# Kernel tuning notes

Measured on AMD Instinct MI355X. Metric: run time of the kernel, lower is better.

## Reference

```python
import jax, jax.numpy as jnp
import numpy as np

S, B, E, H, Q, T, K, N = 256, 32, 768, 1024, 64, 512, 11, 16
STD = 2.5
EPS = 1e-5


def gaussian_kernel(size, std):
    t = np.linspace(-(size - 1) / 2, (size - 1) / 2, size)
    x, y = np.meshgrid(t, t)
    kern = np.exp(-0.5 * (x ** 2 + y ** 2) / std ** 2)
    return (kern / kern.sum()).astype(np.float32)


def setup_inputs() -> dict:
    key = jax.random.key(0)
    ks = jax.random.split(key, 24)
    s = 0.05
    inp = {
        'sentence_batch': jax.random.normal(ks[0], (S, B, E), jnp.float32),
        # forward LSTM params (torch layout: W_ih (4H,E), W_hh (4H,H), gate order i,f,g,o)
        'Wih_f': jax.random.normal(ks[1], (4 * H, E), jnp.float32) * s,
        'Whh_f': jax.random.normal(ks[2], (4 * H, H), jnp.float32) * s,
        'bih_f': jnp.zeros((4 * H,), jnp.float32),
        'bhh_f': jnp.zeros((4 * H,), jnp.float32),
        # backward LSTM params
        'Wih_b': jax.random.normal(ks[3], (4 * H, E), jnp.float32) * s,
        'Whh_b': jax.random.normal(ks[4], (4 * H, H), jnp.float32) * s,
        'bih_b': jnp.zeros((4 * H,), jnp.float32),
        'bhh_b': jnp.zeros((4 * H,), jnp.float32),
        # layer norms
        'g_in': jnp.ones((E,), jnp.float32), 'be_in': jnp.zeros((E,), jnp.float32),
        'g_fw': jnp.ones((H,), jnp.float32), 'be_fw': jnp.zeros((H,), jnp.float32),
        'g_bk': jnp.ones((H,), jnp.float32), 'be_bk': jnp.zeros((H,), jnp.float32),
        'g_sq': jnp.ones((2 * Q,), jnp.float32), 'be_sq': jnp.zeros((2 * Q,), jnp.float32),
        # squeeze + topic linears (torch layout: W (out,in))
        'Wsq': jax.random.normal(ks[5], (Q, H), jnp.float32) * s,
        'bsq': jnp.zeros((Q,), jnp.float32),
        'Wtop': jax.random.normal(ks[6], (T, 2 * Q), jnp.float32) * s,
        'btop': jnp.zeros((T,), jnp.float32),
        'gauss_kern': jnp.asarray(gaussian_kernel(K, STD)),
    }
    return inp


def layer_norm(x, g, b):
    mu = jnp.mean(x, axis=-1, keepdims=True)
    var = jnp.mean((x - mu) ** 2, axis=-1, keepdims=True)
    return g * (x - mu) * jax.lax.rsqrt(var + EPS) + b


def lstm(x, Wih, Whh, bih, bhh):
    # x: (S, B, E) -> hidden states (S, B, H). torch gate order: i, f, g, o.
    h0 = jnp.zeros((x.shape[1], Whh.shape[1]), x.dtype)
    c0 = jnp.zeros_like(h0)
    xg = jnp.einsum('sbe,ge->sbg', x, Wih) + bih  # precompute input gates

    def step(carry, xt):
        h, c = carry
        gates = xt + h @ Whh.T + bhh
        i, f, g, o = jnp.split(gates, 4, axis=-1)
        c = jax.nn.sigmoid(f) * c + jax.nn.sigmoid(i) * jnp.tanh(g)
        h = jax.nn.sigmoid(o) * jnp.tanh(c)
        return (h, c), h

    _, hs = jax.lax.scan(step, (h0, c0), xg)
    return hs


def batch_pca(e, dim):
    # e: (S, B, F) -> projections (B, S, dim) onto top-dim principal axes
    c = e - jnp.mean(e, axis=0)
    cov = jnp.einsum('sbi,sbj->bij', c, c) / e.shape[0]  # (B, F, F), symmetric
    _, evecs = jnp.linalg.eigh(cov)  # ascending eigenvalues
    top = evecs[:, :, ::-1][:, :, :dim]  # (B, F, dim), descending order
    return jnp.einsum('sbf,bfn->bsn', c, top)


def gauss_smooth(x, kern):
    # x: (B, S, N) smoothed with 2D gaussian, SAME padding
    p = (kern.shape[0] - 1) // 2
    y = jax.lax.conv_general_dilated(
        x[:, None, :, :], kern[None, None, :, :], (1, 1), [(p, p), (p, p)])
    return y[:, 0]


def adj_cos(e):
    # cosine similarity between adjacent sequence positions: (B, S, N) -> (B, S-1)
    a, b = e[:, :-1], e[:, 1:]
    num = jnp.sum(a * b, axis=-1)
    den = jnp.linalg.norm(a, axis=-1) * jnp.linalg.norm(b, axis=-1)
    return num / den


def reference(sentence_batch, Wih_f, Whh_f, bih_f, bhh_f, Wih_b, Whh_b, bih_b, bhh_b,
              g_in, be_in, g_fw, be_fw, g_bk, be_bk, g_sq, be_sq,
              Wsq, bsq, Wtop, btop, gauss_kern):
    x = layer_norm(sentence_batch, g_in, be_in)
    x_f = lstm(x, Wih_f, Whh_f, bih_f, bhh_f)
    x_b = lstm(x[::-1], Wih_b, Whh_b, bih_b, bhh_b)[::-1]
    x_f = layer_norm(x_f, g_fw, be_fw)
    x_b = layer_norm(x_b, g_bk, be_bk)
    x_f = jnp.tanh(jnp.einsum('sbh,qh->sbq', x_f, Wsq) + bsq)
    x_b = jnp.tanh(jnp.einsum('sbh,qh->sbq', x_b, Wsq) + bsq)
    xc = layer_norm(jnp.concatenate((x_f, x_b), axis=-1), g_sq, be_sq)
    topic_preds = jnp.einsum('sbq,tq->sbt', xc, Wtop) + btop

    # segmentation path (no-grad in original)
    e_f = batch_pca(jax.lax.stop_gradient(x_f), N)
    e_b = batch_pca(jax.lax.stop_gradient(x_b), N)
    e_f = gauss_smooth(e_f, gauss_kern)
    e_b = gauss_smooth(e_b, gauss_kern)
    d = jnp.sqrt(adj_cos(e_f) * adj_cos(e_b))  # (B, S-1)
    pos = jnp.argmax(d, axis=1)
    return topic_preds, pos
```

## Files before the change

kernel.cpp:

```cpp
#include <hip/hip_runtime.h>
#include <cstdint>
#include <cstddef>

#define SS   256
#define BB   32
#define EE   768
#define HH   1024
#define QQ   64
#define TTOP 512
#define NPC  16
#define G4   4096
#define TCHUNK 32
#define NBLK 256
#define EPSF 1e-5f

#define OFF_XNT   ((size_t)0)
#define OFF_WHHT  ((size_t)6291456)
#define OFF_CT    ((size_t)14680064)
#define OFF_HBUF  ((size_t)14745600)
#define OFF_CNT   ((size_t)14876672)
#define OFF_XG    ((size_t)14877184)
#define OFF_HS    ((size_t)23265792)
#define OFF_XQ    ((size_t)40043008)
#define OFF_CMAT  ((size_t)0)
#define OFF_COV   ((size_t)1048576)
#define OFF_PG    ((size_t)1310720)
#define OFF_COS   ((size_t)1376256)

#define WLKS 4616
#define LSTM_DYN_LDS 153344

#define AST 65
#define EIG_DYN_LDS 133120

#define EPS32D    5.9604644775390625e-8
#define EPS232D   (EPS32D*EPS32D)
#define SAFMIN32D 1.1754943508222875e-38

__device__ __forceinline__ float sigm(float x){ return 1.0f/(1.0f + expf(-x)); }

__device__ __forceinline__ double wsumd(double v){
  #pragma unroll
  for (int o = 32; o; o >>= 1) v += __shfl_xor(v, o, 64);
  return v;
}
__device__ __forceinline__ double wmaxd(double v){
  #pragma unroll
  for (int o = 32; o; o >>= 1) v = fmax(v, __shfl_xor(v, o, 64));
  return v;
}
__device__ __forceinline__ void dlartg_(double f, double g, double& c, double& s, double& r){
  if (g == 0.0){ c = 1.0; s = 0.0; r = f; }
  else if (f == 0.0){ c = 0.0; s = (g >= 0.0) ? 1.0 : -1.0; r = fabs(g); }
  else {
    double d = sqrt(f*f + g*g);
    c = fabs(f)/d;
    r = copysign(d, f);
    s = g/r;
  }
}
__device__ void dlaev2_(double a, double b, double c,
                        double& rt1, double& rt2, double& cs1, double& sn1){
  double sm = a + c, df = a - c, adf = fabs(df), tb = b + b, ab = fabs(tb);
  double acmx, acmn;
  if (fabs(a) > fabs(c)){ acmx = a; acmn = c; } else { acmx = c; acmn = a; }
  double rt;
  if (adf > ab)      rt = adf*sqrt(1.0 + (ab/adf)*(ab/adf));
  else if (adf < ab) rt = ab*sqrt(1.0 + (adf/ab)*(adf/ab));
  else               rt = ab*sqrt(2.0);
  int sgn1;
  if (sm < 0.0){ rt1 = 0.5*(sm - rt); sgn1 = -1; rt2 = (acmx/rt1)*acmn - (b/rt1)*b; }
  else if (sm > 0.0){ rt1 = 0.5*(sm + rt); sgn1 = 1; rt2 = (acmx/rt1)*acmn - (b/rt1)*b; }
  else { rt1 = 0.5*rt; rt2 = -0.5*rt; sgn1 = 1; }
  double cs; int sgn2;
  if (df >= 0.0){ cs = df + rt; sgn2 = 1; } else { cs = df - rt; sgn2 = -1; }
  double acs = fabs(cs);
  if (acs > ab){ double ct = -tb/cs; sn1 = 1.0/sqrt(1.0+ct*ct); cs1 = ct*sn1; }
  else {
    if (ab == 0.0){ cs1 = 1.0; sn1 = 0.0; }
    else { double tn = -cs/tb; cs1 = 1.0/sqrt(1.0+tn*tn); sn1 = tn*cs1; }
  }
  if (sgn1 == sgn2){ double tn = cs1; cs1 = -sn1; sn1 = tn; }
}

__device__ void dsteqr16_(int base, double* d, double* e, double* z16, int ln){
  if (ln < 16){
    #pragma unroll
    for (int j = 0; j < 16; j++) z16[ln*17+j] = (ln==j) ? 1.0 : 0.0;
  }
  __syncthreads();
  const int n = 16, nm1 = 15;
  int jtot = 0; const int nmaxit = 480;
  int l1 = 0;
  while (l1 < n){
    if (l1 > 0) e[base+l1-1] = 0.0;
    int m = nm1;
    for (int mm = l1; mm < nm1; mm++){
      double tst = fabs(e[base+mm]);
      if (tst == 0.0){ m = mm; break; }
      if (tst <= (sqrt(fabs(d[base+mm]))*sqrt(fabs(d[base+mm+1])))*EPS32D){
        e[base+mm] = 0.0; m = mm; break;
      }
    }
    int l = l1, lend = m;
    l1 = m + 1;
    if (lend == l) continue;
    if (fabs(d[base+lend]) < fabs(d[base+l])){ int t = l; l = lend; lend = t; }
    if (lend > l){
      for (;;){
        int mm = lend;
        for (int k2 = l; k2 < lend; k2++){
          double tst = e[base+k2]*e[base+k2];
          if (tst <= (EPS232D*fabs(d[base+k2]))*fabs(d[base+k2+1]) + SAFMIN32D){ mm = k2; break; }
        }
        if (mm < lend) e[base+mm] = 0.0;
        double p = d[base+l];
        if (mm == l){ l++; if (l <= lend) continue; break; }
        if (mm == l+1){
          double rt1, rt2, cc, ss;
          dlaev2_(d[base+l], e[base+l], d[base+l+1], rt1, rt2, cc, ss);
          if (ln < 16){
            double x = z16[ln*17+l], y = z16[ln*17+l+1];
            z16[ln*17+l]   = cc*x + ss*y;
            z16[ln*17+l+1] = cc*y - ss*x;
          }
          d[base+l] = rt1; d[base+l+1] = rt2; e[base+l] = 0.0;
          l += 2; if (l <= lend) continue; break;
        }
        if (jtot == nmaxit) break;
        jtot++;
        double g = (d[base+l+1]-p)/(2.0*e[base+l]);
        double r = sqrt(g*g+1.0);
        g = d[base+mm] - p + e[base+l]/(g + copysign(r, g));
        double s2 = 1.0, c2 = 1.0; p = 0.0;
        for (int i = mm-1; i >= l; i--){
          double f = s2*e[base+i], b = c2*e[base+i];
          dlartg_(g, f, c2, s2, r);
          if (i != mm-1) e[base+i+1] = r;
          g = d[base+i+1] - p;
          r = (d[base+i]-g)*s2 + 2.0*c2*b;
          p = s2*r;
          d[base+i+1] = g + p;
          g = c2*r - b;
          if (ln < 16){
            double x = z16[ln*17+i], y = z16[ln*17+i+1];
            z16[ln*17+i]   = c2*x - s2*y;
            z16[ln*17+i+1] = s2*x + c2*y;
          }
        }
        d[base+l] -= p; e[base+l] = g;
      }
    } else {
      for (;;){
        int mm = lend;
        for (int k2 = l; k2 > lend; k2--){
          double tst = e[base+k2-1]*e[base+k2-1];
          if (tst <= (EPS232D*fabs(d[base+k2]))*fabs(d[base+k2-1]) + SAFMIN32D){ mm = k2; break; }
        }
        if (mm > lend) e[base+mm-1] = 0.0;
        double p = d[base+l];
        if (mm == l){ l--; if (l >= lend) continue; break; }
        if (mm == l-1){
          double rt1, rt2, cc, ss;
          dlaev2_(d[base+l-1], e[base+l-1], d[base+l], rt1, rt2, cc, ss);
          if (ln < 16){
            double x = z16[ln*17+l-1], y = z16[ln*17+l];
            z16[ln*17+l-1] = cc*x + ss*y;
            z16[ln*17+l]   = cc*y - ss*x;
          }
          d[base+l-1] = rt1; d[base+l] = rt2; e[base+l-1] = 0.0;
          l -= 2; if (l >= lend) continue; break;
        }
        if (jtot == nmaxit) break;
        jtot++;
        double g = (d[base+l-1]-p)/(2.0*e[base+l-1]);
        double r = sqrt(g*g+1.0);
        g = d[base+mm] - p + e[base+l-1]/(g + copysign(r, g));
        double s2 = 1.0, c2 = 1.0; p = 0.0;
        for (int i = mm; i <= l-1; i++){
          double f = s2*e[base+i], b = c2*e[base+i];
          dlartg_(g, f, c2, s2, r);
          if (i != mm) e[base+i-1] = r;
          g = d[base+i] - p;
          r = (d[base+i+1]-g)*s2 + 2.0*c2*b;
          p = s2*r;
          d[base+i] = g + p;
          g = c2*r - b;
          if (ln < 16){
            double x = z16[ln*17+i], y = z16[ln*17+i+1];
            z16[ln*17+i]   = c2*x + s2*y;
            z16[ln*17+i+1] = c2*y - s2*x;
          }
        }
        d[base+l] -= p; e[base+l-1] = g;
      }
    }
  }
  for (int ii = 1; ii < n; ii++){
    int i = ii-1, k = i; double p = d[base+i];
    for (int j = ii; j < n; j++) if (d[base+j] < p){ k = j; p = d[base+j]; }
    if (k != i){
      d[base+k] = d[base+i]; d[base+i] = p;
      if (ln < 16){ double t = z16[ln*17+i]; z16[ln*17+i] = z16[ln*17+k]; z16[ln*17+k] = t; }
    }
  }
  __syncthreads();
}

__device__ void dc_merge(int base, int n1, int n2, double rho_in, int ln,
    double* s_d, double* Zt, double* Tt,
    double* md, double* mz, double* dl, double* wz, double* lam, double* zh,
    double* ev, double* su, int* indx, int* sec, int* defl, int* prm){
  int n = n1 + n2;
  double zv = 0.0;
  if (ln < n){
    if (ln < n1) zv = Zt[(size_t)(base+n1-1)*AST + base + ln];
    else         zv = Zt[(size_t)(base+n1)*AST + base + ln];
    if (rho_in < 0.0 && ln >= n1) zv = -zv;
  }
  zv *= 0.70710678118654752440;
  mz[ln] = (ln < n) ? zv : 0.0;
  md[ln] = (ln < n) ? s_d[base+ln] : 0.0;
  __syncthreads();
  double rho = fabs(2.0*rho_in);
  if (ln == 0){
    int i1 = 0, i2 = n1, k = 0;
    while (i1 < n1 && i2 < n){
      if (md[i2] < md[i1]) indx[k++] = i2++; else indx[k++] = i1++;
    }
    while (i1 < n1) indx[k++] = i1++;
    while (i2 < n)  indx[k++] = i2++;
  }
  __syncthreads();
  double dmax = wmaxd((ln<n) ? fabs(md[ln]) : 0.0);
  double zmax = wmaxd((ln<n) ? fabs(mz[ln]) : 0.0);
  double tol = 8.0*EPS32D*fmax(dmax, zmax);
  int K = 0, ndefl = 0, pj = -1;
  for (int j = 0; j < n; j++){
    int nj = indx[j];
    if (rho*fabs(mz[nj]) <= tol){
      defl[ndefl++] = nj;
    } else if (pj < 0){
      pj = nj;
    } else {
      double sG = mz[pj], cG = mz[nj];
      double tau = sqrt(cG*cG + sG*sG);
      double tdf = md[nj] - md[pj];
      double c = cG/tau, s = -sG/tau;
      if (fabs(tdf*c*s) <= tol){
        mz[nj] = tau; mz[pj] = 0.0;
        if (ln < n){
          double x = Zt[(size_t)(base+ln)*AST + base+pj];
          double y = Zt[(size_t)(base+ln)*AST + base+nj];
          Zt[(size_t)(base+ln)*AST + base+pj] = c*x + s*y;
          Zt[(size_t)(base+ln)*AST + base+nj] = c*y - s*x;
        }
        __syncthreads();
        double t2 = md[pj]*c*c + md[nj]*s*s;
        double t3 = md[pj]*s*s + md[nj]*c*c;
        md[nj] = t3; md[pj] = t2;
        defl[ndefl++] = pj;
        pj = nj;
      } else {
        sec[K] = pj; dl[K] = md[pj]; wz[K] = mz[pj]; K++;
        pj = nj;
      }
    }
  }
  if (pj >= 0){ sec[K] = pj; dl[K] = md[pj]; wz[K] = mz[pj]; K++; }
  __syncthreads();
  double wsum2 = wsumd((ln < K) ? wz[ln]*wz[ln] : 0.0);
  if (ln < K){
    double lo = dl[ln];
    double hi = (ln < K-1) ? dl[ln+1] : (dl[K-1] + rho*wsum2);
    for (int it = 0; it < 120; it++){
      double mid = 0.5*(lo+hi);
      if (!(mid > lo) || !(mid < hi)) break;
      double fv = 1.0;
      for (int i2 = 0; i2 < K; i2++) fv += rho*wz[i2]*wz[i2]/(dl[i2]-mid);
      if (fv < 0.0) lo = mid; else hi = mid;
    }
    double lj = 0.5*(lo+hi);
    if (!(lj > dl[ln])) lj = nextafter(dl[ln], 1.0e300);
    lam[ln] = lj;
  }
  __syncthreads();
  if (ln < K){
    double di = dl[ln];
    double prod = lam[K-1] - di;
    for (int j2 = 0; j2 < ln; j2++)   prod *= (lam[j2]-di)/(dl[j2]-di);
    for (int j2 = ln; j2 < K-1; j2++) prod *= (lam[j2]-di)/(dl[j2+1]-di);
    zh[ln] = copysign(sqrt(fabs(prod)), wz[ln]);
  }
  __syncthreads();
  for (int j = 0; j < K; j++){
    double ui = (ln < K) ? zh[ln]/(dl[ln]-lam[j]) : 0.0;
    double nrm = sqrt(wsumd(ui*ui));
    su[ln] = ui/nrm;
    __syncthreads();
    if (ln < n){
      double acc = 0.0;
      for (int i2 = 0; i2 < K; i2++)
        acc += Zt[(size_t)(base+ln)*AST + base + sec[i2]]*su[i2];
      Tt[(size_t)ln*AST + j] = acc;
    }
    if (ln == 0) ev[j] = lam[j];
    __syncthreads();
  }
  for (int j = 0; j < ndefl; j++){
    int cj = defl[j];
    if (ln < n) Tt[(size_t)ln*AST + K + j] = Zt[(size_t)(base+ln)*AST + base + cj];
    if (ln == 0) ev[K+j] = md[cj];
  }
  __syncthreads();
  if (ln == 0){
    for (int i2 = 0; i2 < n; i2++) prm[i2] = i2;
    for (int a2 = 0; a2 < n-1; a2++){
      int kk = a2;
      for (int b2 = a2+1; b2 < n; b2++) if (ev[prm[b2]] < ev[prm[kk]]) kk = b2;
      int t3 = prm[a2]; prm[a2] = prm[kk]; prm[kk] = t3;
    }
  }
  __syncthreads();
  if (ln < n){
    for (int c2 = 0; c2 < n; c2++)
      Zt[(size_t)(base+ln)*AST + base + c2] = Tt[(size_t)ln*AST + prm[c2]];
  }
  if (ln == 0){ for (int c2 = 0; c2 < n; c2++) s_d[base+c2] = ev[prm[c2]]; }
  __syncthreads();
}

__global__ __launch_bounds__(64) void k_eig(const float* __restrict__ covg,
                                            float* __restrict__ Pg){
  int u = blockIdx.x, ln = threadIdx.x;
  extern __shared__ double dsm[];
  double* A  = dsm;
  double* Qh = dsm + 4160;
  double* Zt = dsm + 8320;
  double* Tt = dsm + 12480;
  __shared__ double s_d[64], s_e[64], s_tau[64], s_v[64], s_w[64];
  __shared__ double md[64], mz[64], dl[64], wz[64], lam[64], zh[64], ev[64], su[64];
  __shared__ double z16[16*17];
  __shared__ int indx[64], sec[64], defl[64], prm[64];

  for (int n = ln; n < 4096; n += 64)
    A[(n >> 6)*AST + (n & 63)] = (double)covg[(size_t)u*4096 + n];
  __syncthreads();

  for (int i = 0; i < 63; i++){
    double alpha = A[(size_t)(i+1)*AST + i];
    double xv = (ln >= i+2) ? A[(size_t)ln*AST + i] : 0.0;
    double xnorm2 = wsumd(xv*xv);
    if (xnorm2 == 0.0){
      if (ln == 0){ s_e[i] = alpha; s_tau[i] = 0.0; }
    } else {
      double beta = -copysign(sqrt(alpha*alpha + xnorm2), alpha);
      double taui = (beta - alpha)/beta;
      double sc = 1.0/(alpha - beta);
      s_v[ln] = (ln == i+1) ? 1.0 : ((ln >= i+2) ? A[(size_t)ln*AST+i]*sc : 0.0);
      __syncthreads();
      if (ln >= i+2) A[(size_t)ln*AST+i] = s_v[ln];
      double wr = 0.0;
      if (ln >= i+1){
        for (int c2 = i+1; c2 < 64; c2++){
          double av = (ln >= c2) ? A[(size_t)ln*AST+c2] : A[(size_t)c2*AST+ln];
          wr += av*s_v[c2];
        }
        wr *= taui;
      }
      double dotwv = wsumd((ln >= i+1) ? wr*s_v[ln] : 0.0);
      double alp2 = -0.5*taui*dotwv;
      wr += alp2*s_v[ln];
      s_w[ln] = (ln >= i+1) ? wr : 0.0;
      __syncthreads();
      if (ln >= i+1){
        for (int c2 = i+1; c2 <= ln; c2++)
          A[(size_t)ln*AST+c2] -= s_v[ln]*s_w[c2] + s_w[ln]*s_v[c2];
      }
      if (ln == 0){ s_e[i] = beta; s_tau[i] = taui; }
    }
    __syncthreads();
  }
  s_d[ln] = A[(size_t)ln*AST+ln];
  __syncthreads();

  for (int n = ln; n < 4160; n += 64) Qh[n] = 0.0;
  __syncthreads();
  Qh[(size_t)ln*AST+ln] = 1.0;
  __syncthreads();
  for (int i = 62; i >= 0; i--){
    double taui = s_tau[i];
    if (taui != 0.0){
      s_v[ln] = (ln == i+1) ? 1.0 : ((ln >= i+2) ? A[(size_t)ln*AST+i] : 0.0);
      __syncthreads();
      double dj = 0.0;
      for (int r2 = i+1; r2 < 64; r2++) dj += s_v[r2]*Qh[(size_t)r2*AST+ln];
      dj *= taui;
      for (int r2 = i+1; r2 < 64; r2++) Qh[(size_t)r2*AST+ln] -= s_v[r2]*dj;
    }
    __syncthreads();
  }

  double rho_a = s_e[15], rho_b = s_e[47], rho_top = s_e[31];
  if (ln == 0){
    s_d[15] -= fabs(rho_a);   s_d[16] -= fabs(rho_a);
    s_d[31] -= fabs(rho_top); s_d[32] -= fabs(rho_top);
    s_d[47] -= fabs(rho_b);   s_d[48] -= fabs(rho_b);
  }
  for (int n = ln; n < 4160; n += 64) Zt[n] = 0.0;
  __syncthreads();
  for (int leaf = 0; leaf < 4; leaf++){
    dsteqr16_(leaf*16, s_d, s_e, z16, ln);
    if (ln < 16){
      for (int j = 0; j < 16; j++)
        Zt[(size_t)(leaf*16+ln)*AST + leaf*16 + j] = z16[ln*17+j];
    }
    __syncthreads();
  }
  dc_merge(0, 16, 16, rho_a, ln, s_d, Zt, Tt, md, mz, dl, wz, lam, zh, ev, su, indx, sec, defl, prm);
  dc_merge(32, 16, 16, rho_b, ln, s_d, Zt, Tt, md, mz, dl, wz, lam, zh, ev, su, indx, sec, defl, prm);
  dc_merge(0, 32, 32, rho_top, ln, s_d, Zt, Tt, md, mz, dl, wz, lam, zh, ev, su, indx, sec, defl, prm);

  for (int nn = 0; nn < 16; nn++){
    double acc = 0.0;
    for (int k = 0; k < 64; k++)
      acc += Qh[(size_t)ln*AST+k]*Zt[(size_t)k*AST + (63-nn)];
    Pg[(size_t)u*1024 + ln*16 + nn] = (float)acc;
  }
}

__global__ void k_ln_in(const float* __restrict__ x, const float* __restrict__ g,
                        const float* __restrict__ be, float* __restrict__ xnT){
  int bid = blockIdx.x; int s = bid >> 5, b = bid & 31;
  int tid = threadIdx.x;
  const float* row = x + ((size_t)(s*BB + b))*EE;
  __shared__ float r1[256], r2[256];
  float su = 0.f, sq = 0.f;
  for (int e = tid; e < EE; e += 256){ float v = row[e]; su += v; sq += v*v; }
  r1[tid] = su; r2[tid] = sq; __syncthreads();
  for (int st = 128; st > 0; st >>= 1){
    if (tid < st){ r1[tid] += r1[tid+st]; r2[tid] += r2[tid+st]; }
    __syncthreads();
  }
  float mu  = r1[0] * (1.0f/EE);
  float var = r2[0] * (1.0f/EE) - mu*mu;
  float rstd = rsqrtf(var + EPSF);
  for (int e = tid; e < EE; e += 256){
    float v = (row[e]-mu)*rstd*g[e] + be[e];
    xnT[((size_t)s*EE + e)*BB + b] = v;
  }
}

__global__ void k_whht(const float* __restrict__ Whh_f, const float* __restrict__ Whh_b,
                       float* __restrict__ WhhT){
  int d  = blockIdx.z;
  const float* Whh = d ? Whh_b : Whh_f;
  int rt = blockIdx.x*32, kt = blockIdx.y*32;
  int tx = threadIdx.x & 31, ty = threadIdx.x >> 5;
  __shared__ float tile[32][33];
  for (int i = ty; i < 32; i += 8)
    tile[i][tx] = Whh[(size_t)(rt+i)*HH + kt+tx];
  __syncthreads();
  for (int i = ty; i < 32; i += 8)
    WhhT[((size_t)d*HH + kt+i)*G4 + rt+tx] = tile[tx][i];
}

__global__ void k_zero(float* __restrict__ p, int n){
  int i = blockIdx.x*blockDim.x + threadIdx.x;
  if (i < n) p[i] = 0.f;
}

__global__ __launch_bounds__(256) void k_xg(const float* __restrict__ xnT,
        const float* __restrict__ Wih_f, const float* __restrict__ Wih_b,
        float* __restrict__ xg, int* __restrict__ cnt, int c){
  if (blockIdx.x == 0 && blockIdx.y == 0 && threadIdx.x < 17)
    __hip_atomic_store(&cnt[threadIdx.x*16], 0, __ATOMIC_RELAXED, __HIP_MEMORY_SCOPE_AGENT);
  int nb = blockIdx.x, rb = blockIdx.y;
  int d = rb >> 5, rloc0 = (rb & 31)*128;
  const float* Wih = d ? Wih_b : Wih_f;
  int tid = threadIdx.x;
  int tx = tid & 15, ty = tid >> 4;
  __shared__ float Al[16*132];
  __shared__ float Bl[16*132];
  float acc[8][8];
  #pragma unroll
  for (int i = 0; i < 8; i++)
    #pragma unroll
    for (int j = 0; j < 8; j++) acc[i][j] = 0.f;
  for (int kc = 0; kc < EE; kc += 16){
    #pragma unroll
    for (int j = 0; j < 8; j++){
      int idx = tid + j*256;
      int n = idx & 127, k = idx >> 7;
      int tglob = c*TCHUNK + nb*4 + (n >> 5);
      int tsrc = d ? (SS-1-tglob) : tglob;
      Al[k*132 + n] = xnT[((size_t)tsrc*EE + kc + k)*BB + (n & 31)];
    }
    #pragma unroll
    for (int j = 0; j < 8; j++){
      int idx = tid + j*256;
      int k = idx & 15, r = idx >> 4;
      Bl[k*132 + r] = Wih[(size_t)(rloc0 + r)*EE + kc + k];
    }
    __syncthreads();
    #pragma unroll
    for (int k = 0; k < 16; k++){
      float4 a0 = *(const float4*)(&Al[k*132 + tx*4]);
      float4 a1 = *(const float4*)(&Al[k*132 + 64 + tx*4]);
      float4 b0 = *(const float4*)(&Bl[k*132 + ty*4]);
      float4 b1 = *(const float4*)(&Bl[k*132 + 64 + ty*4]);
      float av[8] = {a0.x,a0.y,a0.z,a0.w,a1.x,a1.y,a1.z,a1.w};
      float bv[8] = {b0.x,b0.y,b0.z,b0.w,b1.x,b1.y,b1.z,b1.w};
      #pragma unroll
      for (int i = 0; i < 8; i++)
        #pragma unroll
        for (int j2 = 0; j2 < 8; j2++) acc[i][j2] += av[i]*bv[j2];
    }
    __syncthreads();
  }
  #pragma unroll
  for (int j = 0; j < 8; j++){
    int r = rloc0 + ((j < 4) ? (ty*4 + j) : (64 + ty*4 + j - 4));
    #pragma unroll
    for (int ig = 0; ig < 2; ig++){
      int n0 = ig*64 + tx*4;
      int tl = nb*4 + (n0 >> 5), b = n0 & 31;
      float4 o = make_float4(acc[ig*4+0][j], acc[ig*4+1][j], acc[ig*4+2][j], acc[ig*4+3][j]);
      *(float4*)(&xg[(((size_t)tl*8192) + d*G4 + r)*BB + b]) = o;
    }
  }
}

__global__ __launch_bounds__(512) void k_lstm(
    const float* __restrict__ WhhT,
    const float* __restrict__ bih_f, const float* __restrict__ bhh_f,
    const float* __restrict__ bih_b, const float* __restrict__ bhh_b,
    const float* __restrict__ xg, float* __restrict__ hbuf,
    float* __restrict__ cT, float* __restrict__ hs,
    int* __restrict__ cnt, int c)
{
  extern __shared__ float lsm[];
  float* Wl  = lsm;
  float* gl  = lsm + 36928;
  float* cls = lsm + 38080;

  const int blk = blockIdx.x;
  const int d   = blk >> 7;
  const int j0  = (blk & 127) * 8;
  const int tid = threadIdx.x;
  const int ln  = tid & 63;
  const int w   = tid >> 6;
  const int ksub = ln >> 3;
  const int bg   = ln & 7;
  const int b0   = bg * 4;
  const int cbase = w * 4;

  const float* bih = d ? bih_b : bih_f;
  const float* bhh = d ? bhh_b : bhh_f;
  const float* WT_d = WhhT + (size_t)d * HH * G4;

  {
    const int cs = tid & 31;
    const int ks = tid >> 5;
    const int g  = cs >> 3, jj = cs & 7;
    const size_t rglob = (size_t)g*HH + j0 + jj;
    for (int kk = 0; kk < 64; kk++){
      int k = kk*16 + ks;
      Wl[(k >> 7)*WLKS + (k & 127)*36 + cs] = WT_d[(size_t)k*G4 + rglob];
    }
  }

  const int pjj = (tid >> 5) & 7, pb = tid & 31;
  float pbias[4];
  if (tid < 256){
    cls[pjj*32 + pb] = cT[((size_t)d*HH + j0 + pjj)*BB + pb];
    #pragma unroll
    for (int g2 = 0; g2 < 4; g2++)
      pbias[g2] = bih[g2*HH + j0 + pjj] + bhh[g2*HH + j0 + pjj];
  }
  __syncthreads();

  for (int tl = 0; tl < TCHUNK; tl++){
    const int s = c*TCHUNK + tl;
    const float* hprev = hbuf + ((size_t)((s & 1)*2 + d))*HH*BB;
    float*       hnext = hbuf + ((size_t)(((s+1) & 1)*2 + d))*HH*BB;

    float xgv[4] = {0.f,0.f,0.f,0.f};
    if (tid < 256){
      const size_t xbase = ((size_t)tl*8192 + (size_t)d*G4)*BB;
      #pragma unroll
      for (int g2 = 0; g2 < 4; g2++)
        xgv[g2] = xg[xbase + (size_t)(g2*HH + j0 + pjj)*BB + pb];
    }

    float acc[4][4];
    #pragma unroll
    for (int i = 0; i < 4; i++)
      #pragma unroll
      for (int j = 0; j < 4; j++) acc[i][j] = 0.f;

    {
      const float* hp = hprev + (size_t)(ksub*128)*BB + b0;
      const float* wrow = &Wl[ksub*WLKS + cbase];
      for (int ib = 0; ib < 128; ib += 16){
        float4 hv[16];
        #pragma unroll
        for (int u = 0; u < 16; u++)
          hv[u] = *(const float4*)(hp + (size_t)(ib+u)*BB);
        #pragma unroll
        for (int u = 0; u < 16; u++){
          float4 wv = *(const float4*)(wrow + (ib+u)*36);
          acc[0][0] += wv.x*hv[u].x; acc[0][1] += wv.x*hv[u].y; acc[0][2] += wv.x*hv[u].z; acc[0][3] += wv.x*hv[u].w;
          acc[1][0] += wv.y*hv[u].x; acc[1][1] += wv.y*hv[u].y; acc[1][2] += wv.y*hv[u].z; acc[1][3] += wv.y*hv[u].w;
          acc[2][0] += wv.z*hv[u].x; acc[2][1] += wv.z*hv[u].y; acc[2][2] += wv.z*hv[u].z; acc[2][3] += wv.z*hv[u].w;
          acc[3][0] += wv.w*hv[u].x; acc[3][1] += wv.w*hv[u].y; acc[3][2] += wv.w*hv[u].z; acc[3][3] += wv.w*hv[u].w;
        }
      }
    }
    #pragma unroll
    for (int i = 0; i < 4; i++)
      #pragma unroll
      for (int j = 0; j < 4; j++){
        float v = acc[i][j];
        v += __shfl_xor(v, 8, 64);
        v += __shfl_xor(v, 16, 64);
        v += __shfl_xor(v, 32, 64);
        acc[i][j] = v;
      }
    if (ksub == 0){
      #pragma unroll
      for (int i = 0; i < 4; i++){
        float4 o = make_float4(acc[i][0], acc[i][1], acc[i][2], acc[i][3]);
        *(float4*)(&gl[(cbase + i)*36 + b0]) = o;
      }
    }
    __syncthreads();
    if (tid < 256){
      float gv[4];
      #pragma unroll
      for (int g2 = 0; g2 < 4; g2++)
        gv[g2] = gl[(g2*8 + pjj)*36 + pb] + pbias[g2] + xgv[g2];
      float iv = sigm(gv[0]), fv = sigm(gv[1]), ggv = tanhf(gv[2]), ov = sigm(gv[3]);
      float cv = fv*cls[pjj*32 + pb] + iv*ggv;
      cls[pjj*32 + pb] = cv;
      float h = ov*tanhf(cv);
      hnext[(size_t)(j0 + pjj)*BB + pb] = h;
      int tsv = d ? (SS-1-s) : s;
      hs[(((size_t)d*SS + tsv)*HH + j0 + pjj)*BB + pb] = h;
    }
    if (tl < TCHUNK-1){
      __syncthreads();
      if (tid == 0){
        __builtin_amdgcn_fence(__ATOMIC_RELEASE, "agent");
        __hip_atomic_fetch_add(&cnt[(blk & 15)*16], 1, __ATOMIC_RELAXED, __HIP_MEMORY_SCOPE_AGENT);
        const int target = 16*(tl+1);
        if (blk == 0){
          int done = 0;
          while (done < 16){
            done = 0;
            #pragma unroll
            for (int i = 0; i < 16; i++)
              done += (__hip_atomic_load(&cnt[i*16], __ATOMIC_RELAXED, __HIP_MEMORY_SCOPE_AGENT) >= target);
            if (done < 16) __builtin_amdgcn_s_sleep(2);
          }
          __hip_atomic_store(&cnt[256], tl+1, __ATOMIC_RELAXED, __HIP_MEMORY_SCOPE_AGENT);
        } else {
          while (__hip_atomic_load(&cnt[256], __ATOMIC_RELAXED, __HIP_MEMORY_SCOPE_AGENT) < tl+1)
            __builtin_amdgcn_s_sleep(2);
        }
        __builtin_amdgcn_fence(__ATOMIC_ACQUIRE, "agent");
      }
      __syncthreads();
    }
  }
  __syncthreads();
  if (tid < 256)
    cT[((size_t)d*HH + j0 + pjj)*BB + pb] = cls[pjj*32 + pb];
}

__global__ __launch_bounds__(256) void k_lnproj(const float* __restrict__ hs,
        const float* __restrict__ g_fw, const float* __restrict__ be_fw,
        const float* __restrict__ g_bk, const float* __restrict__ be_bk,
        const float* __restrict__ Wsq, const float* __restrict__ bsq,
        float* __restrict__ xq){
  int t = blockIdx.x, d = blockIdx.y;
  int tid = threadIdx.x;
  const float* gv  = d ? g_bk  : g_fw;
  const float* bev = d ? be_bk : be_fw;
  const float* hrow = hs + ((size_t)d*SS + t)*HH*BB;
  __shared__ float red[256], red2[256];
  __shared__ float smu[32], srs[32];
  __shared__ float ln[32*132];
  __shared__ float wl[64*132];
  {
    int b = tid & 31, jg = tid >> 5;
    float s = 0.f, s2 = 0.f;
    for (int j = jg*128; j < jg*128+128; j++){
      float v = hrow[(size_t)j*BB + b];
      s += v; s2 += v*v;
    }
    red[b*8 + jg] = s; red2[b*8 + jg] = s2; __syncthreads();
    if (tid < 32){
      float a = 0.f, a2 = 0.f;
      for (int k = 0; k < 8; k++){ a += red[tid*8+k]; a2 += red2[tid*8+k]; }
      float mu = a*(1.f/HH), var = a2*(1.f/HH) - mu*mu;
      smu[tid] = mu; srs[tid] = rsqrtf(var + EPSF);
    }
    __syncthreads();
  }
  float acc[4][2] = {{0.f,0.f},{0.f,0.f},{0.f,0.f},{0.f,0.f}};
  int qg = tid & 31, bg = tid >> 5;
  int q0 = qg*2, b0g = bg*4;
  for (int jc = 0; jc < 8; jc++){
    for (int n = tid; n < 4096; n += 256){
      int b = n & 31, jj = n >> 5; int j = jc*128 + jj;
      float v = hrow[(size_t)j*BB + b];
      ln[b*132+jj] = (v - smu[b])*srs[b]*gv[j] + bev[j];
    }
    for (int n = tid; n < 8192; n += 256){
      int q = n >> 7, jj = n & 127;
      wl[q*132+jj] = Wsq[(size_t)q*HH + jc*128 + jj];
    }
    __syncthreads();
    for (int jj = 0; jj < 128; jj += 4){
      float4 w0 = *(const float4*)(&wl[q0*132+jj]);
      float4 w1 = *(const float4*)(&wl[(q0+1)*132+jj]);
      #pragma unroll
      for (int i = 0; i < 4; i++){
        float4 xv = *(const float4*)(&ln[(b0g+i)*132+jj]);
        acc[i][0] += xv.x*w0.x + xv.y*w0.y + xv.z*w0.z + xv.w*w0.w;
        acc[i][1] += xv.x*w1.x + xv.y*w1.y + xv.z*w1.z + xv.w*w1.w;
      }
    }
    __syncthreads();
  }
  #pragma unroll
  for (int i = 0; i < 4; i++)
    #pragma unroll
    for (int u = 0; u < 2; u++){
      float o = tanhf(acc[i][u] + bsq[q0+u]);
      xq[(((size_t)d*SS + t)*BB + (b0g+i))*QQ + q0 + u] = o;
    }
}

__global__ __launch_bounds__(256) void k_topic(const float* __restrict__ xq,
        const float* __restrict__ g_sq, const float* __restrict__ be_sq,
        const float* __restrict__ Wtop, const float* __restrict__ btop,
        float* __restrict__ out){
  int t = blockIdx.x; int tid = threadIdx.x;
  __shared__ float xc[32*132];
  __shared__ float wl[16*520];
  __shared__ float red[256], red2[256];
  __shared__ float smu[32], srs[32];
  for (int n = tid; n < 4096; n += 256){
    int b = n >> 7, q = n & 127;
    float v = (q < 64) ? xq[(((size_t)0*SS + t)*BB + b)*QQ + q]
                       : xq[(((size_t)1*SS + t)*BB + b)*QQ + (q-64)];
    xc[b*132+q] = v;
  }
  __syncthreads();
// ... 147 lines not shown
}

__global__ void k_pos(const float* __restrict__ cosb, float* __restrict__ out){
  __shared__ float mx[256];
  __shared__ int   mi[256];
  int tid = threadIdx.x;
  for (int b = 0; b < 32; b++){
    float v = -1e30f;
    if (tid < 255){
      float cf = cosb[(size_t)(b)*256 + tid];
      float cb = cosb[(size_t)(32+b)*256 + tid];
      v = sqrtf(cf*cb);
      if (isnan(v)) v = INFINITY;
    }
    mx[tid] = v; __syncthreads();
    for (int st = 128; st > 0; st >>= 1){
      if (tid < st) mx[tid] = fmaxf(mx[tid], mx[tid+st]);
      __syncthreads();
    }
    float m = mx[0]; __syncthreads();
    mi[tid] = (tid < 255 && v == m) ? tid : (1<<30);
    __syncthreads();
    for (int st = 128; st > 0; st >>= 1){
      if (tid < st) mi[tid] = min(mi[tid], mi[tid+st]);
      __syncthreads();
    }
    if (tid == 0) out[(size_t)SS*BB*TTOP + b] = (float)mi[0];
    __syncthreads();
  }
}

extern "C" void kernel_launch(void* const* d_in, const int* in_sizes, int n_in,
                              void* d_out, int out_size, void* d_ws, size_t ws_size,
                              hipStream_t stream){
  (void)in_sizes; (void)n_in; (void)out_size; (void)ws_size;
  const float* x      = (const float*)d_in[0];
  const float* Wih_f  = (const float*)d_in[1];
  const float* Whh_f  = (const float*)d_in[2];
  const float* bih_f  = (const float*)d_in[3];
  const float* bhh_f  = (const float*)d_in[4];
  const float* Wih_b  = (const float*)d_in[5];
  const float* Whh_b  = (const float*)d_in[6];
  const float* bih_b  = (const float*)d_in[7];
  const float* bhh_b  = (const float*)d_in[8];
  const float* g_in   = (const float*)d_in[9];
  const float* be_in  = (const float*)d_in[10];
  const float* g_fw   = (const float*)d_in[11];
  const float* be_fw  = (const float*)d_in[12];
  const float* g_bk   = (const float*)d_in[13];
  const float* be_bk  = (const float*)d_in[14];
  const float* g_sq   = (const float*)d_in[15];
  const float* be_sq  = (const float*)d_in[16];
  const float* Wsq    = (const float*)d_in[17];
  const float* bsq    = (const float*)d_in[18];
  const float* Wtop   = (const float*)d_in[19];
  const float* btop   = (const float*)d_in[20];
  const float* gkern  = (const float*)d_in[21];

  float* ws    = (float*)d_ws;
  float* xnT   = ws + OFF_XNT;
  float* WhhT  = ws + OFF_WHHT;
  float* cT    = ws + OFF_CT;
  float* hbuf  = ws + OFF_HBUF;
  int*   cnt   = (int*)(ws + OFF_CNT);
  float* xg    = ws + OFF_XG;
  float* hs    = ws + OFF_HS;
  float* xq    = ws + OFF_XQ;
  float* cmat  = ws + OFF_CMAT;
  float* covg  = ws + OFF_COV;
  float* Pg    = ws + OFF_PG;
  float* cosb  = ws + OFF_COS;
  float* out   = (float*)d_out;

  hipFuncSetAttribute((const void*)k_eig,
                      hipFuncAttributeMaxDynamicSharedMemorySize, EIG_DYN_LDS);
  hipFuncSetAttribute((const void*)k_lstm,
                      hipFuncAttributeMaxDynamicSharedMemorySize, LSTM_DYN_LDS);

  k_zero<<<dim3(768), dim3(256), 0, stream>>>(cT, 196608);
  k_ln_in<<<dim3(SS*BB), dim3(256), 0, stream>>>(x, g_in, be_in, xnT);
  k_whht<<<dim3(128, 32, 2), dim3(256), 0, stream>>>(Whh_f, Whh_b, WhhT);
  for (int c = 0; c < SS/TCHUNK; c++){
    k_xg<<<dim3(8, 64), dim3(256), 0, stream>>>(xnT, Wih_f, Wih_b, xg, cnt, c);
    k_lstm<<<dim3(NBLK), dim3(512), LSTM_DYN_LDS, stream>>>(WhhT, bih_f, bhh_f, bih_b, bhh_b,
                                                            xg, hbuf, cT, hs, cnt, c);
  }
  k_lnproj<<<dim3(SS,2), dim3(256), 0, stream>>>(hs, g_fw, be_fw, g_bk, be_bk, Wsq, bsq, xq);
  k_topic<<<dim3(SS), dim3(256), 0, stream>>>(xq, g_sq, be_sq, Wtop, btop, out);
  k_pca1<<<dim3(64), dim3(256), 0, stream>>>(xq, cmat, covg);
  k_eig<<<dim3(64), dim3(64), EIG_DYN_LDS, stream>>>(covg, Pg);
  k_pca2<<<dim3(64), dim3(256), 0, stream>>>(cmat, Pg, gkern, cosb);
  k_pos<<<dim3(1), dim3(256), 0, stream>>>(cosb, out);
}
```

Baseline: 8.312 ms.

## Restructure LSTM recurrence to 256 threads and parallelize eigensolver across four waves

The LSTM step kernel drops from 512 to 256 threads. Each wave now covers a 256-wide k-range for all 32 gate columns, and partial sums are combined through an LDS tree reduction instead of cross-lane shuffles, so the idle upper half of the block during the gate update goes away. The eigen kernel moves from 64 to 256 threads: the four 16x16 leaf QR solves run concurrently, one per wave, the secular-vector columns in the merge step are split across waves, and the Householder updates are split across waves by column. The trade-offs are fewer threads hiding latency in the LSTM and extra barriers in the reduction.

```diff
diff --git a/kernel.cpp b/kernel.cpp
--- a/kernel.cpp
+++ b/kernel.cpp
@@ -28,7 +28,7 @@
 #define OFF_COS   ((size_t)1376256)
 
 #define WLKS 4616
-#define LSTM_DYN_LDS 153344
+#define LSTM_DYN_LDS 161536
 
 #define AST 65
 #define EIG_DYN_LDS 133120
@@ -88,7 +88,6 @@
     #pragma unroll
     for (int j = 0; j < 16; j++) z16[ln*17+j] = (ln==j) ? 1.0 : 0.0;
   }
-  __syncthreads();
   const int n = 16, nm1 = 15;
   int jtot = 0; const int nmaxit = 480;
   int l1 = 0;
@@ -204,13 +203,14 @@
       if (ln < 16){ double t = z16[ln*17+i]; z16[ln*17+i] = z16[ln*17+k]; z16[ln*17+k] = t; }
     }
   }
-  __syncthreads();
-}
-
-__device__ void dc_merge(int base, int n1, int n2, double rho_in, int ln,
+}
+
+__device__ void dc_merge(int base, int n1, int n2, double rho_in, int tid,
     double* s_d, double* Zt, double* Tt,
     double* md, double* mz, double* dl, double* wz, double* lam, double* zh,
-    double* ev, double* su, int* indx, int* sec, int* defl, int* prm){
+    double* ev, double* su4, int* indx, int* sec, int* defl, int* prm,
+    int* sKn){
+  const int ln = tid & 63, w = tid >> 6;
   int n = n1 + n2;
   double zv = 0.0;
   if (ln < n){
@@ -223,7 +223,7 @@
   md[ln] = (ln < n) ? s_d[base+ln] : 0.0;
   __syncthreads();
   double rho = fabs(2.0*rho_in);
-  if (ln == 0){
+  if (tid == 0){
     int i1 = 0, i2 = n1, k = 0;
     while (i1 < n1 && i2 < n){
       if (md[i2] < md[i1]) indx[k++] = i2++; else indx[k++] = i1++;
@@ -235,40 +235,43 @@
   double dmax = wmaxd((ln<n) ? fabs(md[ln]) : 0.0);
   double zmax = wmaxd((ln<n) ? fabs(mz[ln]) : 0.0);
   double tol = 8.0*EPS32D*fmax(dmax, zmax);
-  int K = 0, ndefl = 0, pj = -1;
-  for (int j = 0; j < n; j++){
-    int nj = indx[j];
-    if (rho*fabs(mz[nj]) <= tol){
-      defl[ndefl++] = nj;
-    } else if (pj < 0){
-      pj = nj;
-    } else {
-      double sG = mz[pj], cG = mz[nj];
-      double tau = sqrt(cG*cG + sG*sG);
-      double tdf = md[nj] - md[pj];
-      double c = cG/tau, s = -sG/tau;
-      if (fabs(tdf*c*s) <= tol){
-        mz[nj] = tau; mz[pj] = 0.0;
-        if (ln < n){
-          double x = Zt[(size_t)(base+ln)*AST + base+pj];
-          double y = Zt[(size_t)(base+ln)*AST + base+nj];
-          Zt[(size_t)(base+ln)*AST + base+pj] = c*x + s*y;
-          Zt[(size_t)(base+ln)*AST + base+nj] = c*y - s*x;
-        }
-        __syncthreads();
-        double t2 = md[pj]*c*c + md[nj]*s*s;
-        double t3 = md[pj]*s*s + md[nj]*c*c;
-        md[nj] = t3; md[pj] = t2;
-        defl[ndefl++] = pj;
+  if (w == 0){
+    int K = 0, ndefl = 0, pj = -1;
+    for (int j = 0; j < n; j++){
+      int nj = indx[j];
+      if (rho*fabs(mz[nj]) <= tol){
+        defl[ndefl++] = nj;
+      } else if (pj < 0){
         pj = nj;
       } else {
-        sec[K] = pj; dl[K] = md[pj]; wz[K] = mz[pj]; K++;
-        pj = nj;
-      }
-    }
-  }
-  if (pj >= 0){ sec[K] = pj; dl[K] = md[pj]; wz[K] = mz[pj]; K++; }
-  __syncthreads();
+        double sG = mz[pj], cG = mz[nj];
+        double tau = sqrt(cG*cG + sG*sG);
+        double tdf = md[nj] - md[pj];
+        double c = cG/tau, s = -sG/tau;
+        if (fabs(tdf*c*s) <= tol){
+          mz[nj] = tau; mz[pj] = 0.0;
+          if (ln < n){
+            double x = Zt[(size_t)(base+ln)*AST + base+pj];
+            double y = Zt[(size_t)(base+ln)*AST + base+nj];
+            Zt[(size_t)(base+ln)*AST + base+pj] = c*x + s*y;
+            Zt[(size_t)(base+ln)*AST + base+nj] = c*y - s*x;
+          }
+          double t2 = md[pj]*c*c + md[nj]*s*s;
+          double t3 = md[pj]*s*s + md[nj]*c*c;
+          md[nj] = t3; md[pj] = t2;
+          defl[ndefl++] = pj;
+          pj = nj;
+        } else {
+          sec[K] = pj; dl[K] = md[pj]; wz[K] = mz[pj]; K++;
+          pj = nj;
+        }
+      }
+    }
+    if (pj >= 0){ sec[K] = pj; dl[K] = md[pj]; wz[K] = mz[pj]; K++; }
+    if (ln == 0){ sKn[0] = K; sKn[1] = ndefl; }
+  }
+  __syncthreads();
+  const int K = sKn[0], ndefl = sKn[1];
   double wsum2 = wsumd((ln < K) ? wz[ln]*wz[ln] : 0.0);
   if (ln < K){
     double lo = dl[ln];
@@ -293,27 +296,26 @@
     zh[ln] = copysign(sqrt(fabs(prod)), wz[ln]);
   }
   __syncthreads();
-  for (int j = 0; j < K; j++){
+  for (int j = w; j < K; j += 4){
     double ui = (ln < K) ? zh[ln]/(dl[ln]-lam[j]) : 0.0;
     double nrm = sqrt(wsumd(ui*ui));
-    su[ln] = ui/nrm;
-    __syncthreads();
+    su4[w*64 + ln] = ui/nrm;
     if (ln < n){
       double acc = 0.0;
       for (int i2 = 0; i2 < K; i2++)
-        acc += Zt[(size_t)(base+ln)*AST + base + sec[i2]]*su[i2];
+        acc += Zt[(size_t)(base+ln)*AST + base + sec[i2]]*su4[w*64 + i2];
       Tt[(size_t)ln*AST + j] = acc;
     }
     if (ln == 0) ev[j] = lam[j];
-    __syncthreads();
-  }
+  }
+  __syncthreads();
   for (int j = 0; j < ndefl; j++){
     int cj = defl[j];
     if (ln < n) Tt[(size_t)ln*AST + K + j] = Zt[(size_t)(base+ln)*AST + base + cj];
     if (ln == 0) ev[K+j] = md[cj];
   }
   __syncthreads();
-  if (ln == 0){
+  if (tid == 0){
     for (int i2 = 0; i2 < n; i2++) prm[i2] = i2;
     for (int a2 = 0; a2 < n-1; a2++){
       int kk = a2;
@@ -330,20 +332,22 @@
   __syncthreads();
 }
 
-__global__ __launch_bounds__(64) void k_eig(const float* __restrict__ covg,
-                                            float* __restrict__ Pg){
-  int u = blockIdx.x, ln = threadIdx.x;
+__global__ __launch_bounds__(256) void k_eig(const float* __restrict__ covg,
+                                             float* __restrict__ Pg){
+  int u = blockIdx.x, tid = threadIdx.x;
+  const int ln = tid & 63, w = tid >> 6;
   extern __shared__ double dsm[];
   double* A  = dsm;
   double* Qh = dsm + 4160;
   double* Zt = dsm + 8320;
   double* Tt = dsm + 12480;
   __shared__ double s_d[64], s_e[64], s_tau[64], s_v[64], s_w[64];
-  __shared__ double md[64], mz[64], dl[64], wz[64], lam[64], zh[64], ev[64], su[64];
-  __shared__ double z16[16*17];
-  __shared__ int indx[64], sec[64], defl[64], prm[64];
-
-  for (int n = ln; n < 4096; n += 64)
+  __shared__ double md[64], mz[64], dl[64], wz[64], lam[64], zh[64], ev[64];
+  __shared__ double su4[4*64];
+  __shared__ double z16a[4*272];
+  __shared__ int indx[64], sec[64], defl[64], prm[64], sKn[2];
+
+  for (int n = tid; n < 4096; n += 256)
     A[(n >> 6)*AST + (n & 63)] = (double)covg[(size_t)u*4096 + n];
   __syncthreads();
 
@@ -352,7 +356,7 @@
     double xv = (ln >= i+2) ? A[(size_t)ln*AST + i] : 0.0;
     double xnorm2 = wsumd(xv*xv);
     if (xnorm2 == 0.0){
-      if (ln == 0){ s_e[i] = alpha; s_tau[i] = 0.0; }
+      if (tid == 0){ s_e[i] = alpha; s_tau[i] = 0.0; }
     } else {
       double beta = -copysign(sqrt(alpha*alpha + xnorm2), alpha);
       double taui = (beta - alpha)/beta;
@@ -375,18 +379,19 @@
       __syncthreads();
       if (ln >= i+1){
         for (int c2 = i+1; c2 <= ln; c2++)
-          A[(size_t)ln*AST+c2] -= s_v[ln]*s_w[c2] + s_w[ln]*s_v[c2];
-      }
-      if (ln == 0){ s_e[i] = beta; s_tau[i] = taui; }
-    }
-    __syncthreads();
-  }
-  s_d[ln] = A[(size_t)ln*AST+ln];
-  __syncthreads();
-
-  for (int n = ln; n < 4160; n += 64) Qh[n] = 0.0;
-  __syncthreads();
-  Qh[(size_t)ln*AST+ln] = 1.0;
+          if ((c2 & 3) == w)
+            A[(size_t)ln*AST+c2] -= s_v[ln]*s_w[c2] + s_w[ln]*s_v[c2];
+      }
+      if (tid == 0){ s_e[i] = beta; s_tau[i] = taui; }
+    }
+    __syncthreads();
+  }
+  if (w == 0) s_d[ln] = A[(size_t)ln*AST+ln];
+  __syncthreads();
+
+  for (int n = tid; n < 4160; n += 256) Qh[n] = 0.0;
+  __syncthreads();
+  if (w == 0) Qh[(size_t)ln*AST+ln] = 1.0;
   __syncthreads();
   for (int i = 62; i >= 0; i--){
     double taui = s_tau[i];
@@ -396,32 +401,33 @@
       double dj = 0.0;
       for (int r2 = i+1; r2 < 64; r2++) dj += s_v[r2]*Qh[(size_t)r2*AST+ln];
       dj *= taui;
-      for (int r2 = i+1; r2 < 64; r2++) Qh[(size_t)r2*AST+ln] -= s_v[r2]*dj;
+      for (int r2 = i+1; r2 < 64; r2++)
+        if ((r2 & 3) == w)
+          Qh[(size_t)r2*AST+ln] -= s_v[r2]*dj;
     }
     __syncthreads();
   }
 
   double rho_a = s_e[15], rho_b = s_e[47], rho_top = s_e[31];
-  if (ln == 0){
+  if (tid == 0){
     s_d[15] -= fabs(rho_a);   s_d[16] -= fabs(rho_a);
     s_d[31] -= fabs(rho_top); s_d[32] -= fabs(rho_top);
     s_d[47] -= fabs(rho_b);   s_d[48] -= fabs(rho_b);
   }
-  for (int n = ln; n < 4160; n += 64) Zt[n] = 0.0;
-  __syncthreads();
-  for (int leaf = 0; leaf < 4; leaf++){
-    dsteqr16_(leaf*16, s_d, s_e, z16, ln);
-    if (ln < 16){
-      for (int j = 0; j < 16; j++)
-        Zt[(size_t)(leaf*16+ln)*AST + leaf*16 + j] = z16[ln*17+j];
-    }
-    __syncthreads();
-  }
-  dc_merge(0, 16, 16, rho_a, ln, s_d, Zt, Tt, md, mz, dl, wz, lam, zh, ev, su, indx, sec, defl, prm);
-  dc_merge(32, 16, 16, rho_b, ln, s_d, Zt, Tt, md, mz, dl, wz, lam, zh, ev, su, indx, sec, defl, prm);
-  dc_merge(0, 32, 32, rho_top, ln, s_d, Zt, Tt, md, mz, dl, wz, lam, zh, ev, su, indx, sec, defl, prm);
-
-  for (int nn = 0; nn < 16; nn++){
+  for (int n = tid; n < 4160; n += 256) Zt[n] = 0.0;
+  __syncthreads();
+  dsteqr16_(w*16, s_d, s_e, &z16a[w*272], ln);
+  if (ln < 16){
+    for (int j = 0; j < 16; j++)
+      Zt[(size_t)(w*16+ln)*AST + w*16 + j] = z16a[w*272 + ln*17+j];
+  }
+  __syncthreads();
+
+  dc_merge(0, 16, 16, rho_a, tid, s_d, Zt, Tt, md, mz, dl, wz, lam, zh, ev, su4, indx, sec, defl, prm, sKn);
+  dc_merge(32, 16, 16, rho_b, tid, s_d, Zt, Tt, md, mz, dl, wz, lam, zh, ev, su4, indx, sec, defl, prm, sKn);
+  dc_merge(0, 32, 32, rho_top, tid, s_d, Zt, Tt, md, mz, dl, wz, lam, zh, ev, su4, indx, sec, defl, prm, sKn);
+
+  for (int nn = w; nn < 16; nn += 4){
     double acc = 0.0;
     for (int k = 0; k < 64; k++)
       acc += Qh[(size_t)ln*AST+k]*Zt[(size_t)k*AST + (63-nn)];
@@ -531,7 +537,7 @@
   }
 }
 
-__global__ __launch_bounds__(512) void k_lstm(
+__global__ __launch_bounds__(256) void k_lstm(
     const float* __restrict__ WhhT,
     const float* __restrict__ bih_f, const float* __restrict__ bhh_f,
     const float* __restrict__ bih_b, const float* __restrict__ bhh_b,
@@ -541,8 +547,9 @@
 {
   extern __shared__ float lsm[];
   float* Wl  = lsm;
-  float* gl  = lsm + 36928;
-  float* cls = lsm + 38080;
+  float* red = lsm + 36928;
+  float* gl  = lsm + 38976;
+  float* cls = lsm + 40128;
 
   const int blk = blockIdx.x;
   const int d   = blk >> 7;
@@ -550,10 +557,10 @@
   const int tid = threadIdx.x;
   const int ln  = tid & 63;
   const int w   = tid >> 6;
-  const int ksub = ln >> 3;
-  const int bg   = ln & 7;
-  const int b0   = bg * 4;
-  const int cbase = w * 4;
+  const int cg  = ln >> 3;
+  const int bg  = ln & 7;
+  const int b0  = bg * 4;
+  const int cbase = cg * 4;
 
   const float* bih = d ? bih_b : bih_f;
   const float* bhh = d ? bhh_b : bhh_f;
@@ -564,20 +571,18 @@
     const int ks = tid >> 5;
     const int g  = cs >> 3, jj = cs & 7;
     const size_t rglob = (size_t)g*HH + j0 + jj;
-    for (int kk = 0; kk < 64; kk++){
-      int k = kk*16 + ks;
+    for (int kk = 0; kk < 128; kk++){
+      int k = kk*8 + ks;
       Wl[(k >> 7)*WLKS + (k & 127)*36 + cs] = WT_d[(size_t)k*G4 + rglob];
     }
   }
 
-  const int pjj = (tid >> 5) & 7, pb = tid & 31;
+  const int pjj = tid >> 5, pb = tid & 31;
+  cls[pjj*32 + pb] = cT[((size_t)d*HH + j0 + pjj)*BB + pb];
   float pbias[4];
-  if (tid < 256){
-    cls[pjj*32 + pb] = cT[((size_t)d*HH + j0 + pjj)*BB + pb];
-    #pragma unroll
-    for (int g2 = 0; g2 < 4; g2++)
-      pbias[g2] = bih[g2*HH + j0 + pjj] + bhh[g2*HH + j0 + pjj];
-  }
+  #pragma unroll
+  for (int g2 = 0; g2 < 4; g2++)
+    pbias[g2] = bih[g2*HH + j0 + pjj] + bhh[g2*HH + j0 + pjj];
   __syncthreads();
 
   for (int tl = 0; tl < TCHUNK; tl++){
@@ -585,8 +590,8 @@
     const float* hprev = hbuf + ((size_t)((s & 1)*2 + d))*HH*BB;
     float*       hnext = hbuf + ((size_t)(((s+1) & 1)*2 + d))*HH*BB;
 
-    float xgv[4] = {0.f,0.f,0.f,0.f};
-    if (tid < 256){
+    float xgv[4];
+    {
       const size_t xbase = ((size_t)tl*8192 + (size_t)d*G4)*BB;
       #pragma unroll
       for (int g2 = 0; g2 < 4; g2++)
@@ -600,16 +605,16 @@
       for (int j = 0; j < 4; j++) acc[i][j] = 0.f;
 
     {
-      const float* hp = hprev + (size_t)(ksub*128)*BB + b0;
-      const float* wrow = &Wl[ksub*WLKS + cbase];
-      for (int ib = 0; ib < 128; ib += 16){
+      const float* hp = hprev + (size_t)(w*256)*BB + b0;
+      for (int ib = 0; ib < 256; ib += 16){
         float4 hv[16];
         #pragma unroll
         for (int u = 0; u < 16; u++)
           hv[u] = *(const float4*)(hp + (size_t)(ib+u)*BB);
         #pragma unroll
         for (int u = 0; u < 16; u++){
-          float4 wv = *(const float4*)(wrow + (ib+u)*36);
+          int k = w*256 + ib + u;
+          float4 wv = *(const float4*)(&Wl[(k >> 7)*WLKS + (k & 127)*36 + cbase]);
           acc[0][0] += wv.x*hv[u].x; acc[0][1] += wv.x*hv[u].y; acc[0][2] += wv.x*hv[u].z; acc[0][3] += wv.x*hv[u].w;
           acc[1][0] += wv.y*hv[u].x; acc[1][1] += wv.y*hv[u].y; acc[1][2] += wv.y*hv[u].z; acc[1][3] += wv.y*hv[u].w;
           acc[2][0] += wv.z*hv[u].x; acc[2][1] += wv.z*hv[u].y; acc[2][2] += wv.z*hv[u].z; acc[2][3] += wv.z*hv[u].w;
@@ -617,25 +622,42 @@
         }
       }
     }
-    #pragma unroll
-    for (int i = 0; i < 4; i++)
-      #pragma unroll
-      for (int j = 0; j < 4; j++){
-        float v = acc[i][j];
-        v += __shfl_xor(v, 8, 64);
-        v += __shfl_xor(v, 16, 64);
-        v += __shfl_xor(v, 32, 64);
-        acc[i][j] = v;
-      }
-    if (ksub == 0){
+    if (w == 1 || w == 3){
+      float* rp = &red[(w >> 1)*1024 + ln*16];
+      #pragma unroll
+      for (int i = 0; i < 4; i++)
+        #pragma unroll
+        for (int j = 0; j < 4; j++) rp[i*4+j] = acc[i][j];
+    }
+    __syncthreads();
+    if (w == 0 || w == 2){
+      const float* rp = &red[(w >> 1)*1024 + ln*16];
+      #pragma unroll
+      for (int i = 0; i < 4; i++)
+        #pragma unroll
+        for (int j = 0; j < 4; j++) acc[i][j] += rp[i*4+j];
+    }
+    __syncthreads();
+    if (w == 2){
+      float* rp = &red[ln*16];
+      #pragma unroll
+      for (int i = 0; i < 4; i++)
+        #pragma unroll
+        for (int j = 0; j < 4; j++) rp[i*4+j] = acc[i][j];
+    }
+    __syncthreads();
+    if (w == 0){
+      const float* rp = &red[ln*16];
       #pragma unroll
       for (int i = 0; i < 4; i++){
+        #pragma unroll
+        for (int j = 0; j < 4; j++) acc[i][j] += rp[i*4+j];
         float4 o = make_float4(acc[i][0], acc[i][1], acc[i][2], acc[i][3]);
         *(float4*)(&gl[(cbase + i)*36 + b0]) = o;
       }
     }
     __syncthreads();
-    if (tid < 256){
+    {
       float gv[4];
       #pragma unroll
       for (int g2 = 0; g2 < 4; g2++)
@@ -674,8 +696,7 @@
     }
   }
   __syncthreads();
-  if (tid < 256)
-    cT[((size_t)d*HH + j0 + pjj)*BB + pb] = cls[pjj*32 + pb];
+  cT[((size_t)d*HH + j0 + pjj)*BB + pb] = cls[pjj*32 + pb];
 }
 
 __global__ __launch_bounds__(256) void k_lnproj(const float* __restrict__ hs,
@@ -989,13 +1010,13 @@
   k_whht<<<dim3(128, 32, 2), dim3(256), 0, stream>>>(Whh_f, Whh_b, WhhT);
   for (int c = 0; c < SS/TCHUNK; c++){
     k_xg<<<dim3(8, 64), dim3(256), 0, stream>>>(xnT, Wih_f, Wih_b, xg, cnt, c);
-    k_lstm<<<dim3(NBLK), dim3(512), LSTM_DYN_LDS, stream>>>(WhhT, bih_f, bhh_f, bih_b, bhh_b,
+    k_lstm<<<dim3(NBLK), dim3(256), LSTM_DYN_LDS, stream>>>(WhhT, bih_f, bhh_f, bih_b, bhh_b,
                                                             xg, hbuf, cT, hs, cnt, c);
   }
   k_lnproj<<<dim3(SS,2), dim3(256), 0, stream>>>(hs, g_fw, be_fw, g_bk, be_bk, Wsq, bsq, xq);
   k_topic<<<dim3(SS), dim3(256), 0, stream>>>(xq, g_sq, be_sq, Wtop, btop, out);
   k_pca1<<<dim3(64), dim3(256), 0, stream>>>(xq, cmat, covg);
-  k_eig<<<dim3(64), dim3(64), EIG_DYN_LDS, stream>>>(covg, Pg);
+  k_eig<<<dim3(64), dim3(256), EIG_DYN_LDS, stream>>>(covg, Pg);
   k_pca2<<<dim3(64), dim3(256), 0, stream>>>(cmat, Pg, gkern, cosb);
   k_pos<<<dim3(1), dim3(256), 0, stream>>>(cosb, out);
 }
```

Measured after the change: 9.021 ms. +8.5%, slower.
